# Optimization experiments

Hardware: AMD Instinct MI355X
Metric: run time of the kernel (lower is better)

Reference implementation:

```python
import jax, jax.numpy as jnp
import numpy as np

ROUTINGS = 3
NUM_CAPSULE = 32
DIM_CAPSULE = 32
EPS_KERAS = 1e-7   # K.epsilon()
EPS_L2 = 1e-12     # tf.nn.l2_normalize epsilon


def squash(x, axis=-1):
    s2 = jnp.sum(jnp.square(x), axis=axis, keepdims=True)
    return (s2 / (1.0 + s2)) * x / jnp.sqrt(s2 + EPS_KERAS)


def l2_normalize(x, axis=-1):
    s2 = jnp.sum(jnp.square(x), axis=axis, keepdims=True)
    return x * jax.lax.rsqrt(jnp.maximum(s2, EPS_L2))


def setup_inputs() -> dict:
    key = jax.random.key(0)
    k1, k2 = jax.random.split(key)
    u_vecs = jax.random.normal(k1, (32, 2048, 16), dtype=jnp.float32)
    # glorot-like small scale for the local kernel to keep routing numerics sane
    W = jax.random.normal(k2, (2048, 16, NUM_CAPSULE * DIM_CAPSULE), dtype=jnp.float32) * 0.05
    return {"u_vecs": u_vecs, "W": W}


def reference(u_vecs, W):
    B, N_in, _ = u_vecs.shape
    # local_conv1d with kernel size 1 == per-input-capsule matmul
    u_hat = jnp.einsum('bni,nio->bno', u_vecs, W)
    # [B, N_in, num_cap, dim] -> [B, num_cap, N_in, dim]
    u_hat = u_hat.reshape(B, N_in, NUM_CAPSULE, DIM_CAPSULE).transpose(0, 2, 1, 3)
    b = jnp.zeros((B, NUM_CAPSULE, N_in), dtype=u_hat.dtype)
    o = None
    for i in range(ROUTINGS):
        c = jax.nn.softmax(b, axis=1)              # softmax over output capsules
        o = jnp.einsum('bin,binj->bij', c, u_hat)  # [B, num_cap, dim]
        if i < ROUTINGS - 1:
            o = l2_normalize(o, axis=-1)
            b = jnp.einsum('bij,binj->bin', o, u_hat)
    return squash(o, axis=-1)
```

## Files before the change

kernel.cpp:

```cpp
#include <hip/hip_runtime.h>
#include <math.h>
#include <stdint.h>

#define BB   32
#define HB   16
#define NN   2048
#define KK   16
#define CC   32
#define DD   32
#define NCOL 1024
#define NPB  8
#define WT   (KK * NCOL)
#define OSZ  (BB * NCOL)
#define NSLICE 8

__device__ __forceinline__ void dma16(const float* g, const float* l) {
    __builtin_amdgcn_global_load_lds(
        (const __attribute__((address_space(1))) void*)(uintptr_t)g,
        (__attribute__((address_space(3))) void*)(uintptr_t)l,
        16, 0, 0);
}

__global__ __launch_bounds__(1024)
void caps_stage(const float* __restrict__ u, const float* __restrict__ W,
                const float* __restrict__ onorm, float* __restrict__ part)
{
    __shared__ float Wt[WT];
    __shared__ float ush[NPB * KK * HB];
    __shared__ float logit_sh[HB * CC];
    __shared__ float c_sh[HB * CC];

    const int tid  = threadIdx.x;
    const int wave = tid >> 6;
    const int lane = tid & 63;
    const int bg = tid >> 8;
    const int cq = tid & 255;
    const int i0 = cq >> 3;
    const int jq = cq & 7;
    const int b0 = bg << 2;
    const int c0 = cq << 2;

    const int ngrp  = blockIdx.x >> 1;
    const int bhalf = blockIdx.x & 1;
    const int n0    = ngrp * NPB;
    const int bbase = bhalf * HB;

    const int woff = wave << 10;
    const int loff = lane << 2;

    auto dma_tile = [&](int n) {
        const float* g = W + (size_t)n * WT + woff + loff;
        const float* l = &Wt[woff];
#pragma unroll
        for (int j = 0; j < 4; ++j)
            dma16(g + j * 256, l + j * 256);
    };

    dma_tile(n0);
    for (int idx = tid; idx < NPB * KK * HB; idx += 1024) {
        const int n = idx >> 8, rem = idx & 255, k = rem >> 4, b = rem & 15;
        ush[idx] = u[(size_t)(bbase + b) * (NN * KK) + (size_t)(n0 + n) * KK + k];
    }
    __syncthreads();

    float opart[4][4];
#pragma unroll
    for (int bb = 0; bb < 4; ++bb)
#pragma unroll
        for (int m = 0; m < 4; ++m) opart[bb][m] = 0.f;

    for (int nn = 0; nn < NPB; ++nn) {
        const float* un = &ush[nn << 8];

        float accU[4][4];
#pragma unroll
        for (int bb = 0; bb < 4; ++bb)
#pragma unroll
            for (int m = 0; m < 4; ++m) accU[bb][m] = 0.f;

#pragma unroll
        for (int k = 0; k < KK; ++k) {
            const float4 w  = *(const float4*)&Wt[k * NCOL + c0];
            const float4 ub = *(const float4*)&un[(k << 4) + b0];
            accU[0][0] = fmaf(ub.x, w.x, accU[0][0]);
            accU[0][1] = fmaf(ub.x, w.y, accU[0][1]);
            accU[0][2] = fmaf(ub.x, w.z, accU[0][2]);
            accU[0][3] = fmaf(ub.x, w.w, accU[0][3]);
            accU[1][0] = fmaf(ub.y, w.x, accU[1][0]);
            accU[1][1] = fmaf(ub.y, w.y, accU[1][1]);
            accU[1][2] = fmaf(ub.y, w.z, accU[1][2]);
            accU[1][3] = fmaf(ub.y, w.w, accU[1][3]);
            accU[2][0] = fmaf(ub.z, w.x, accU[2][0]);
            accU[2][1] = fmaf(ub.z, w.y, accU[2][1]);
            accU[2][2] = fmaf(ub.z, w.z, accU[2][2]);
            accU[2][3] = fmaf(ub.z, w.w, accU[2][3]);
            accU[3][0] = fmaf(ub.w, w.x, accU[3][0]);
            accU[3][1] = fmaf(ub.w, w.y, accU[3][1]);
            accU[3][2] = fmaf(ub.w, w.z, accU[3][2]);
            accU[3][3] = fmaf(ub.w, w.w, accU[3][3]);
        }

        float lp[4];
#pragma unroll
        for (int bb = 0; bb < 4; ++bb) {
            const float4 on4 = *(const float4*)(
                onorm + ((size_t)(bbase + b0 + bb) * CC + i0) * DD + (jq << 2));
            float p = accU[bb][0] * on4.x + accU[bb][1] * on4.y
                    + accU[bb][2] * on4.z + accU[bb][3] * on4.w;
            p += __shfl_xor(p, 1);
            p += __shfl_xor(p, 2);
            p += __shfl_xor(p, 4);
            lp[bb] = p;
        }
        if (jq == 0) {
#pragma unroll
            for (int bb = 0; bb < 4; ++bb)
                logit_sh[(b0 + bb) * CC + i0] = lp[bb];
        }
        __syncthreads();

        {
            int np = n0 + nn + 1;
            if (np >= NN) np = NN - 1;
            dma_tile(np);
        }

        if (tid < HB * CC) {
            const int b  = tid >> 5;
            const int ii = tid & 31;
            float l = logit_sh[b * CC + ii];
            float mx = l;
#pragma unroll
            for (int msk = 16; msk >= 1; msk >>= 1)
                mx = fmaxf(mx, __shfl_xor(mx, msk));
            const float e = __expf(l - mx);
            float sm = e;
#pragma unroll
            for (int msk = 16; msk >= 1; msk >>= 1)
                sm += __shfl_xor(sm, msk);
            c_sh[b * CC + ii] = e / sm;
        }
        __syncthreads();

#pragma unroll
        for (int bb = 0; bb < 4; ++bb) {
            const float cc = c_sh[(b0 + bb) * CC + i0];
#pragma unroll
            for (int m = 0; m < 4; ++m)
                opart[bb][m] = fmaf(cc, accU[bb][m], opart[bb][m]);
        }
    }

    float* my = part + (size_t)ngrp * OSZ + (size_t)bbase * NCOL;
#pragma unroll
    for (int bb = 0; bb < 4; ++bb) {
        float4 v;
        v.x = opart[bb][0]; v.y = opart[bb][1];
        v.z = opart[bb][2]; v.w = opart[bb][3];
        *(float4*)&my[(b0 + bb) * NCOL + c0] = v;
    }
}

__global__ __launch_bounds__(256) void caps_reduce1(
    const float* __restrict__ part, float* __restrict__ ws2)
{
    const int gid   = blockIdx.x * 256 + threadIdx.x;
    const int slice = gid >> 13;
    const int q     = gid & 8191;
    float4 acc = make_float4(0.f, 0.f, 0.f, 0.f);
    const float* p = part + ((size_t)slice * 32) * OSZ + (q << 2);
#pragma unroll 8
    for (int j = 0; j < 32; ++j) {
        const float4 v = *(const float4*)(p + (size_t)j * OSZ);
        acc.x += v.x; acc.y += v.y; acc.z += v.z; acc.w += v.w;
    }
    *(float4*)(ws2 + ((size_t)gid << 2)) = acc;
}

__global__ __launch_bounds__(256) void caps_reduce2(
    const float* __restrict__ ws2, float* __restrict__ dst, int mode)
{
    const int q = blockIdx.x * 256 + threadIdx.x;
    float4 acc = make_float4(0.f, 0.f, 0.f, 0.f);
#pragma unroll
    for (int s = 0; s < NSLICE; ++s) {
        const float4 v = *(const float4*)(ws2 + ((size_t)s << 15) + (q << 2));
        acc.x += v.x; acc.y += v.y; acc.z += v.z; acc.w += v.w;
    }
    float s2 = acc.x * acc.x + acc.y * acc.y + acc.z * acc.z + acc.w * acc.w;
    s2 += __shfl_xor(s2, 1);
    s2 += __shfl_xor(s2, 2);
    s2 += __shfl_xor(s2, 4);
    float scale;
    if (mode == 0) {
        scale = rsqrtf(fmaxf(s2, 1e-12f));
    } else {
        scale = (s2 / (1.f + s2)) / sqrtf(s2 + 1e-7f);
    }
    float4 o;
    o.x = acc.x * scale; o.y = acc.y * scale;
    o.z = acc.z * scale; o.w = acc.w * scale;
    *(float4*)(dst + ((size_t)q << 2)) = o;
}

extern "C" void kernel_launch(void* const* d_in, const int* in_sizes, int n_in,
                              void* d_out, int out_size, void* d_ws, size_t ws_size,
                              hipStream_t stream)
{
    const float* u = (const float*)d_in[0];
    const float* W = (const float*)d_in[1];
    float* out = (float*)d_out;

    float* part  = (float*)d_ws;
    float* ws2   = part + (size_t)256 * OSZ;
    float* onorm = ws2 + (size_t)NSLICE * OSZ;

    hipMemsetAsync(onorm, 0, (size_t)OSZ * sizeof(float), stream);

    for (int it = 0; it < 3; ++it) {
        caps_stage<<<2 * (NN / NPB), 1024, 0, stream>>>(u, W, onorm, part);
        caps_reduce1<<<256, 256, 0, stream>>>(part, ws2);
        if (it < 2)
            caps_reduce2<<<32, 256, 0, stream>>>(ws2, onorm, 0);
        else
            caps_reduce2<<<32, 256, 0, stream>>>(ws2, out, 1);
    }
}
```

Baseline: 392.9 us.

## Split W tile into two halves and double-buffer the LDS DMA prefetch

The per-input-capsule W tile in LDS is split into two 8-row halves. Each half is prefetched into its own buffer as soon as its readers are done, so the next tile's loads overlap the second half of the matmul and the routing-softmax section. The redundant prefetch after the last tile is dropped. This adds one extra block barrier per input capsule and assumes the existing barriers also wait for the LDS-DMA to finish.

```diff
diff --git a/kernel.cpp b/kernel.cpp
--- a/kernel.cpp
+++ b/kernel.cpp
@@ -11,6 +11,7 @@
 #define NCOL 1024
 #define NPB  8
 #define WT   (KK * NCOL)
+#define WH   (8 * NCOL)
 #define OSZ  (BB * NCOL)
 #define NSLICE 8
 
@@ -25,7 +26,7 @@
 void caps_stage(const float* __restrict__ u, const float* __restrict__ W,
                 const float* __restrict__ onorm, float* __restrict__ part)
 {
-    __shared__ float Wt[WT];
+    __shared__ float Wh[2][WH];
     __shared__ float ush[NPB * KK * HB];
     __shared__ float logit_sh[HB * CC];
     __shared__ float c_sh[HB * CC];
@@ -45,23 +46,23 @@
     const int n0    = ngrp * NPB;
     const int bbase = bhalf * HB;
 
-    const int woff = wave << 10;
+    const int woff = wave << 9;
     const int loff = lane << 2;
 
-    auto dma_tile = [&](int n) {
-        const float* g = W + (size_t)n * WT + woff + loff;
-        const float* l = &Wt[woff];
-#pragma unroll
-        for (int j = 0; j < 4; ++j)
-            dma16(g + j * 256, l + j * 256);
+    auto dma_half = [&](int n, int half, int buf) {
+        const float* g = W + (size_t)n * WT + half * WH + woff + loff;
+        const float* l = &Wh[buf][woff];
+        dma16(g, l);
+        dma16(g + 256, l + 256);
     };
 
-    dma_tile(n0);
+    dma_half(n0, 0, 0);
     for (int idx = tid; idx < NPB * KK * HB; idx += 1024) {
         const int n = idx >> 8, rem = idx & 255, k = rem >> 4, b = rem & 15;
         ush[idx] = u[(size_t)(bbase + b) * (NN * KK) + (size_t)(n0 + n) * KK + k];
     }
     __syncthreads();
+    dma_half(n0, 1, 1);
 
     float opart[4][4];
 #pragma unroll
@@ -71,6 +72,8 @@
 
     for (int nn = 0; nn < NPB; ++nn) {
         const float* un = &ush[nn << 8];
+        const int np = n0 + nn + 1;
+        const bool pf = (nn + 1 < NPB);
 
         float accU[4][4];
 #pragma unroll
@@ -79,8 +82,8 @@
             for (int m = 0; m < 4; ++m) accU[bb][m] = 0.f;
 
 #pragma unroll
-        for (int k = 0; k < KK; ++k) {
-            const float4 w  = *(const float4*)&Wt[k * NCOL + c0];
+        for (int k = 0; k < 8; ++k) {
+            const float4 w  = *(const float4*)&Wh[0][k * NCOL + c0];
             const float4 ub = *(const float4*)&un[(k << 4) + b0];
             accU[0][0] = fmaf(ub.x, w.x, accU[0][0]);
             accU[0][1] = fmaf(ub.x, w.y, accU[0][1]);
@@ -100,30 +103,52 @@
             accU[3][3] = fmaf(ub.w, w.w, accU[3][3]);
         }
 
-        float lp[4];
-#pragma unroll
-        for (int bb = 0; bb < 4; ++bb) {
-            const float4 on4 = *(const float4*)(
-                onorm + ((size_t)(bbase + b0 + bb) * CC + i0) * DD + (jq << 2));
-            float p = accU[bb][0] * on4.x + accU[bb][1] * on4.y
-                    + accU[bb][2] * on4.z + accU[bb][3] * on4.w;
-            p += __shfl_xor(p, 1);
-            p += __shfl_xor(p, 2);
-            p += __shfl_xor(p, 4);
-            lp[bb] = p;
-        }
-        if (jq == 0) {
-#pragma unroll
-            for (int bb = 0; bb < 4; ++bb)
-                logit_sh[(b0 + bb) * CC + i0] = lp[bb];
-        }
         __syncthreads();
 
+        if (pf) dma_half(np, 0, 0);
+
+#pragma unroll
+        for (int k = 0; k < 8; ++k) {
+            const float4 w  = *(const float4*)&Wh[1][k * NCOL + c0];
+            const float4 ub = *(const float4*)&un[((k + 8) << 4) + b0];
+            accU[0][0] = fmaf(ub.x, w.x, accU[0][0]);
+            accU[0][1] = fmaf(ub.x, w.y, accU[0][1]);
+            accU[0][2] = fmaf(ub.x, w.z, accU[0][2]);
+            accU[0][3] = fmaf(ub.x, w.w, accU[0][3]);
+            accU[1][0] = fmaf(ub.y, w.x, accU[1][0]);
+            accU[1][1] = fmaf(ub.y, w.y, accU[1][1]);
+            accU[1][2] = fmaf(ub.y, w.z, accU[1][2]);
+            accU[1][3] = fmaf(ub.y, w.w, accU[1][3]);
+            accU[2][0] = fmaf(ub.z, w.x, accU[2][0]);
+            accU[2][1] = fmaf(ub.z, w.y, accU[2][1]);
+            accU[2][2] = fmaf(ub.z, w.z, accU[2][2]);
+            accU[2][3] = fmaf(ub.z, w.w, accU[2][3]);
+            accU[3][0] = fmaf(ub.w, w.x, accU[3][0]);
+            accU[3][1] = fmaf(ub.w, w.y, accU[3][1]);
+            accU[3][2] = fmaf(ub.w, w.z, accU[3][2]);
+            accU[3][3] = fmaf(ub.w, w.w, accU[3][3]);
+        }
+
         {
-            int np = n0 + nn + 1;
-            if (np >= NN) np = NN - 1;
-            dma_tile(np);
-        }
+            float lp[4];
+#pragma unroll
+            for (int bb = 0; bb < 4; ++bb) {
+                const float4 on4 = *(const float4*)(
+                    onorm + ((size_t)(bbase + b0 + bb) * CC + i0) * DD + (jq << 2));
+                float p = accU[bb][0] * on4.x + accU[bb][1] * on4.y
+                        + accU[bb][2] * on4.z + accU[bb][3] * on4.w;
+                p += __shfl_xor(p, 1);
+                p += __shfl_xor(p, 2);
+                p += __shfl_xor(p, 4);
+                lp[bb] = p;
+            }
+            if (jq == 0) {
+#pragma unroll
+                for (int bb = 0; bb < 4; ++bb)
+                    logit_sh[(b0 + bb) * CC + i0] = lp[bb];
+            }
+        }
+        __syncthreads();
 
         if (tid < HB * CC) {
             const int b  = tid >> 5;
@@ -149,6 +174,7 @@
             for (int m = 0; m < 4; ++m)
                 opart[bb][m] = fmaf(cc, accU[bb][m], opart[bb][m]);
         }
+        if (pf) dma_half(np, 1, 1);
     }
 
     float* my = part + (size_t)ngrp * OSZ + (size_t)bbase * NCOL;
```

New measurement: 536.5 us. +36.6%, slower.
